# Performance work log

Measured on AMD Instinct MI355X. Metric: run time of the kernel, lower is better.

The kernel has to match this reference:

```python
import jax, jax.numpy as jnp
import numpy as np

NEG = 1e9  # large negative bias used by the original code for masked positions


def setup_inputs() -> dict:
    key = jax.random.key(0)
    k1, k2, k3 = jax.random.split(key, 3)
    B, H, W, Ck, Cv = 8, 64, 64, 64, 128
    return {
        "query": jax.random.normal(k1, (B, H, W, Ck), dtype=jnp.float32),
        "key": jax.random.normal(k2, (B, H, W, Ck), dtype=jnp.float32),
        "value": jax.random.normal(k3, (B, H, W, Cv), dtype=jnp.float32),
    }


def reference(query, key, value):
    B, Hq, Wq, Ck = query.shape
    Cv = value.shape[-1]
    Nq = Hq * Wq                      # query canvas size
    Nk = key.shape[1] * key.shape[2]  # key/value canvas size

    q = query.reshape(B, Nq, Ck)
    k = key.reshape(B, Nk, Ck)
    v = value.reshape(B, Nk, Cv)

    # strictly-causal pixelSNAIL mask: pixel i may attend only to pixels j < i
    allowed = jnp.tril(jnp.ones((Nq, Nk), dtype=query.dtype), k=-1)

    # [B, Nq, Nk] scaled dot-product scores
    scores = jnp.einsum("bqc,bkc->bqk", q, k) / jnp.sqrt(jnp.asarray(Ck, query.dtype))
    scores = scores - NEG * (1.0 - allowed)

    # softmax then redundant re-mask (as in the original module)
    probs = jax.nn.softmax(scores, axis=-1) * allowed

    out = jnp.einsum("bqk,bkv->bqv", probs, v)
    return out.reshape(B, Hq, Wq, Cv)
```

## Files before the change

kernel.cpp:

```cpp
#include <hip/hip_runtime.h>
#include <hip/hip_bf16.h>

typedef unsigned short u16;
typedef unsigned int u32;
typedef __attribute__((ext_vector_type(2))) unsigned int u32x2;
typedef __attribute__((ext_vector_type(4))) unsigned int u32x4;
typedef __attribute__((ext_vector_type(4))) float f32x4;
typedef __attribute__((ext_vector_type(8))) short bf16x8;
typedef __attribute__((ext_vector_type(16))) float f32x16;

typedef __attribute__((address_space(1))) const void as1_cvoid;
typedef __attribute__((address_space(3))) void as3_void;

__device__ __forceinline__ u32 cvtpk(float lo, float hi) {
    __hip_bfloat162 h = __float22bfloat162_rn(make_float2(lo, hi));
    u32 r; __builtin_memcpy(&r, &h, 4);
    return r;
}
__device__ __forceinline__ int crow(int r, int hl) { return (r & 3) + 8 * (r >> 2) + 4 * hl; }

#define NROW 4096
#define CK 64
#define CV 128
#define TILE_U16 24576
#define WS_NEEDED (8u * 32u * 49152u)
#define SWK(R, o) ((((R) << 7) + (o)) ^ (((R) & 7) << 4))
#define SWVG(R) ((((R) >> 3) & 15) ^ (((R) & 7) << 1))
#define SWV(R, o) ((((R) << 8) + (o)) ^ (SWVG(R) << 4))

__global__ __launch_bounds__(512, 2) void prep_k(const float* __restrict__ Kg,
                                                 const float* __restrict__ Vg,
                                                 u16* __restrict__ ws) {
    int bid = blockIdx.x;
    int b = bid >> 5, jt = bid & 31;
    int t = threadIdx.x;
    int jK = t >> 2, kc4 = t & 3;
    int vg = t & 15, jgrp = t >> 4;
    const float* Kp = Kg + ((size_t)b * NROW + jt * 128) * CK;
    const float* Vp = Vg + ((size_t)b * NROW + jt * 128) * CV;
    u16* img = ws + (size_t)(b * 32 + jt) * TILE_U16;

    {
        const float* kp = Kp + (size_t)jK * CK + kc4 * 16;
        f32x4 a0 = *(const f32x4*)kp,       a1 = *(const f32x4*)(kp + 4);
        f32x4 a2 = *(const f32x4*)(kp + 8), a3 = *(const f32x4*)(kp + 12);
        u32x4 kk0, kk1;
        kk0[0] = cvtpk(a0[0], a0[1]); kk0[1] = cvtpk(a0[2], a0[3]);
        kk0[2] = cvtpk(a1[0], a1[1]); kk0[3] = cvtpk(a1[2], a1[3]);
        kk1[0] = cvtpk(a2[0], a2[1]); kk1[1] = cvtpk(a2[2], a2[3]);
        kk1[2] = cvtpk(a3[0], a3[1]); kk1[3] = cvtpk(a3[2], a3[3]);
        *(u32x4*)&img[SWK(jK, kc4 * 32) >> 1]      = kk0;
        *(u32x4*)&img[SWK(jK, kc4 * 32 + 16) >> 1] = kk1;
    }
    {
        const float* vp = Vp + (size_t)(jgrp * 4) * CV + vg * 8;
        f32x4 va0 = *(const f32x4*)vp,            vb0 = *(const f32x4*)(vp + 4);
        f32x4 va1 = *(const f32x4*)(vp + CV),     vb1 = *(const f32x4*)(vp + CV + 4);
        f32x4 va2 = *(const f32x4*)(vp + 2 * CV), vb2 = *(const f32x4*)(vp + 2 * CV + 4);
        f32x4 va3 = *(const f32x4*)(vp + 3 * CV), vb3 = *(const f32x4*)(vp + 3 * CV + 4);
#pragma unroll
        for (int x = 0; x < 4; x++) {
            u32x2 vv;
            vv[0] = cvtpk(va0[x], va1[x]); vv[1] = cvtpk(va2[x], va3[x]);
            *(u32x2*)&img[8192 + (SWV(vg * 8 + x, jgrp * 8) >> 1)] = vv;
            vv[0] = cvtpk(vb0[x], vb1[x]); vv[1] = cvtpk(vb2[x], vb3[x]);
            *(u32x2*)&img[8192 + (SWV(vg * 8 + 4 + x, jgrp * 8) >> 1)] = vv;
        }
    }
}

__global__ __launch_bounds__(512, 2) void attn_m(const float* __restrict__ Qg,
                                                 const u16* __restrict__ ws,
                                                 float* __restrict__ O) {
    __shared__ __align__(16) u16 smem[2 * TILE_U16 + 16512];

    int bid = blockIdx.x;
    int bb = bid & 7;
    int u  = bid >> 3;
    int t  = threadIdx.x;
    int w  = t >> 6;
    int lane = t & 63;
    int ql = lane & 31, hl = lane >> 5;
    int qsub = w >> 2;
    int jq   = w & 3;
    int uL = u, uH = 63 - u;
    int NR1 = ((2 * uL + 1) >> 2) + 1;
    int NR2 = 33 - NR1;

    const float* Qp = Qg + (size_t)bb * NROW * CK;
    const u16* imgB = ws + (size_t)bb * 32 * TILE_U16;
    const float qscale = 0.125f * 1.44269504088896f;

    bf16x8 qf[4];
    auto loadQ = [&](int T) {
        const float* qb = Qp + (size_t)((T << 5) + ql) * CK;
#pragma unroll
        for (int kc = 0; kc < 4; kc++) {
            const float* qp = qb + kc * 16 + hl * 8;
            f32x4 a = *(const f32x4*)qp;
            f32x4 b2 = *(const f32x4*)(qp + 4);
            u32x4 qq;
            qq[0] = cvtpk(a[0] * qscale, a[1] * qscale);
            qq[1] = cvtpk(a[2] * qscale, a[3] * qscale);
            qq[2] = cvtpk(b2[0] * qscale, b2[1] * qscale);
            qq[3] = cvtpk(b2[2] * qscale, b2[3] * qscale);
            qf[kc] = __builtin_bit_cast(bf16x8, qq);
        }
    };
    int T_cur = 2 * uL + qsub;
    loadQ(T_cur);

    f32x16 acc[4];
#pragma unroll
    for (int vs = 0; vs < 4; vs++)
#pragma unroll
        for (int r = 0; r < 16; r++) acc[vs][r] = 0.f;
    float l = 0.f;

    auto issueTile = [&](int img_tile, int buf_u16) {
        const char* src = (const char*)(imgB + (size_t)img_tile * TILE_U16)
                          + w * 6144 + lane * 16;
        char* dst = (char*)smem + (size_t)buf_u16 * 2 + w * 6144;
#pragma unroll
        for (int i = 0; i < 6; i++)
            __builtin_amdgcn_global_load_lds((as1_cvoid*)(src + i * 1024),
                                             (as3_void*)(dst + i * 1024), 16, 0, 0);
    };

    auto combine = [&](int Tq) {
        float* cm = (float*)&smem[2 * TILE_U16];
        float* lA = cm + 8192;
        float lw = l + __shfl_xor(l, 32);
        if (jq == 0) {
#pragma unroll
            for (int vs = 0; vs < 4; vs++)
#pragma unroll
                for (int r = 0; r < 16; r++)
                    cm[qsub * 4096 + crow(r, hl) * 128 + vs * 32 + ql] = acc[vs][r];
            if (lane < 32) lA[qsub * 32 + lane] = lw;
        }
        __syncthreads();
        if (jq == 1) {
#pragma unroll
            for (int vs = 0; vs < 4; vs++)
#pragma unroll
                for (int r = 0; r < 16; r++)
                    cm[qsub * 4096 + crow(r, hl) * 128 + vs * 32 + ql] += acc[vs][r];
            if (lane < 32) lA[qsub * 32 + lane] += lw;
        }
        __syncthreads();
        if (jq == 2) {
#pragma unroll
            for (int vs = 0; vs < 4; vs++)
#pragma unroll
                for (int r = 0; r < 16; r++)
                    cm[qsub * 4096 + crow(r, hl) * 128 + vs * 32 + ql] += acc[vs][r];
            if (lane < 32) lA[qsub * 32 + lane] += lw;
        }
        __syncthreads();
        if (jq == 3) {
            float ltot = lA[qsub * 32 + ql] + lw;
            float inv = ((Tq << 5) + ql == 0) ? 0.f : 1.f / ltot;
            float inv_r[16];
#pragma unroll
            for (int r = 0; r < 16; r++) inv_r[r] = __shfl(inv, crow(r, hl));
            float* Og = O + ((size_t)bb * NROW + ((size_t)Tq << 5)) * CV;
#pragma unroll
            for (int vs = 0; vs < 4; vs++)
#pragma unroll
                for (int r = 0; r < 16; r++)
                    Og[(size_t)crow(r, hl) * CV + vs * 32 + ql] =
                        (cm[qsub * 4096 + crow(r, hl) * 128 + vs * 32 + ql] + acc[vs][r]) * inv_r[r];
        }
        __syncthreads();
    };

    issueTile(0, 0);

    for (int rr = 0; rr < 33; ++rr) {
        int cur = (rr & 1) * TILE_U16;
        int nxt = ((rr + 1) & 1) * TILE_U16;

        {
            int nr = rr + 1;
            int jb = (nr < NR1) ? nr : (nr - NR1 < NR2 ? nr - NR1 : NR2 - 1);
            issueTile(jb, nxt);
        }
        asm volatile("s_waitcnt vmcnt(6)" ::: "memory");
        __builtin_amdgcn_sched_barrier(0);
        __builtin_amdgcn_s_barrier();

        if (rr == NR1) {
            combine(T_cur);
#pragma unroll
            for (int vs = 0; vs < 4; vs++)
#pragma unroll
                for (int r = 0; r < 16; r++) acc[vs][r] = 0.f;
            l = 0.f;
            T_cur = 2 * uH + qsub;
            loadQ(T_cur);
        }

        int tt = (rr < NR1) ? rr : rr - NR1;
        int jS = 4 * tt + jq;
        if (jS <= T_cur) {
            bf16x8 kf0 = *(const bf16x8*)&smem[cur + (SWK(jq * 32 + ql, 0 * 32 + hl * 16) >> 1)];
            bf16x8 kf1 = *(const bf16x8*)&smem[cur + (SWK(jq * 32 + ql, 1 * 32 + hl * 16) >> 1)];
            bf16x8 kf2 = *(const bf16x8*)&smem[cur + (SWK(jq * 32 + ql, 2 * 32 + hl * 16) >> 1)];
            bf16x8 kf3 = *(const bf16x8*)&smem[cur + (SWK(jq * 32 + ql, 3 * 32 + hl * 16) >> 1)];

            f32x16 Sa, Sb;
#pragma unroll
            for (int r = 0; r < 16; r++) { Sa[r] = 0.f; Sb[r] = 0.f; }
            __builtin_amdgcn_s_setprio(1);
            Sa = __builtin_amdgcn_mfma_f32_32x32x16_bf16(kf0, qf[0], Sa, 0, 0, 0);
            Sb = __builtin_amdgcn_mfma_f32_32x32x16_bf16(kf2, qf[2], Sb, 0, 0, 0);
            Sa = __builtin_amdgcn_mfma_f32_32x32x16_bf16(kf1, qf[1], Sa, 0, 0, 0);
            Sb = __builtin_amdgcn_mfma_f32_32x32x16_bf16(kf3, qf[3], Sb, 0, 0, 0);
            __builtin_amdgcn_s_setprio(0);

            float P[16];
            bool diag = (jS == T_cur);
#pragma unroll
            for (int r = 0; r < 16; r++) {
                float pr2 = __builtin_exp2f(Sa[r] + Sb[r]);
                if (diag) pr2 = (crow(r, hl) >= ql) ? 0.f : pr2;
                P[r] = pr2;
            }
            {
                float s0 = (P[0] + P[1]) + (P[2] + P[3]);
                float s1 = (P[4] + P[5]) + (P[6] + P[7]);
                float s2 = (P[8] + P[9]) + (P[10] + P[11]);
                float s3 = (P[12] + P[13]) + (P[14] + P[15]);
                l += (s0 + s1) + (s2 + s3);
            }

            u32 A0 = cvtpk(P[0], P[1]),   B0 = cvtpk(P[2], P[3]);
            u32 A1 = cvtpk(P[4], P[5]),   B1 = cvtpk(P[6], P[7]);
            u32 A2 = cvtpk(P[8], P[9]),   B2 = cvtpk(P[10], P[11]);
            u32 A3 = cvtpk(P[12], P[13]), B3 = cvtpk(P[14], P[15]);
            u32 s1 = hl ? A0 : A1, s2 = hl ? B0 : B1;
            u32 s3 = hl ? A2 : A3, s4 = hl ? B2 : B3;
            u32 r1 = (u32)__shfl_xor((int)s1, 32);
            u32 r2 = (u32)__shfl_xor((int)s2, 32);
            u32 r3 = (u32)__shfl_xor((int)s3, 32);
            u32 r4 = (u32)__shfl_xor((int)s4, 32);

            bf16x8 vf0[4], vf1[4];
#pragma unroll
            for (int vs = 0; vs < 4; vs++) {
                vf0[vs] = *(const bf16x8*)&smem[cur + 8192 + (SWV(vs * 32 + ql, jq * 64 + hl * 16) >> 1)];
                vf1[vs] = *(const bf16x8*)&smem[cur + 8192 + (SWV(vs * 32 + ql, jq * 64 + 32 + hl * 16) >> 1)];
            }
            u32x4 w0, w1;
            w0[0] = hl ? r1 : A0; w0[1] = hl ? r2 : B0;
            w0[2] = hl ? A1 : r1; w0[3] = hl ? B1 : r2;
            w1[0] = hl ? r3 : A2; w1[1] = hl ? r4 : B2;
            w1[2] = hl ? A3 : r3; w1[3] = hl ? B3 : r4;
            bf16x8 pa0 = __builtin_bit_cast(bf16x8, w0);
            bf16x8 pa1 = __builtin_bit_cast(bf16x8, w1);

            __builtin_amdgcn_s_setprio(1);
#pragma unroll
            for (int vs = 0; vs < 4; vs++)
                acc[vs] = __builtin_amdgcn_mfma_f32_32x32x16_bf16(pa0, vf0[vs], acc[vs], 0, 0, 0);
#pragma unroll
            for (int vs = 0; vs < 4; vs++)
                acc[vs] = __builtin_amdgcn_mfma_f32_32x32x16_bf16(pa1, vf1[vs], acc[vs], 0, 0, 0);
            __builtin_amdgcn_s_setprio(0);
        }
        __builtin_amdgcn_s_barrier();
    }

    combine(T_cur);
}

#define FBUF 24576
#define FVT 8192
__global__ __launch_bounds__(512, 2) void attn_fb(const float* __restrict__ Qg,
                                                  const float* __restrict__ Kg,
                                                  const float* __restrict__ Vg,
                                                  float* __restrict__ O) {
    __shared__ __align__(16) u16 smem[2 * FBUF];
    int bid = blockIdx.x;
    int bb = bid & 7;
    int u  = bid >> 3;
    int t  = threadIdx.x;
    int w  = t >> 6;
    int lane = t & 63;
    int ql = lane & 31, hl = lane >> 5;
    int qsub = w >> 2, jq = w & 3;
    int uL = u, uH = 63 - u;
    int rA = ((2 * uL + 1) >> 2) + 1;
    const float* Qp = Qg + (size_t)bb * NROW * CK;
    const float* Kp = Kg + (size_t)bb * NROW * CK;
    const float* Vp = Vg + (size_t)bb * NROW * CV;
    const float qscale = 0.125f * 1.44269504088896f;
    bf16x8 qf[4];
    auto loadQ = [&](int T) {
        const float* qb = Qp + (size_t)((T << 5) + ql) * CK;
#pragma unroll
        for (int kc = 0; kc < 4; kc++) {
            const float* qp = qb + kc * 16 + hl * 8;
            f32x4 a = *(const f32x4*)qp;
            f32x4 b2 = *(const f32x4*)(qp + 4);
            u32x4 qq;
            qq[0] = cvtpk(a[0] * qscale, a[1] * qscale);
            qq[1] = cvtpk(a[2] * qscale, a[3] * qscale);
            qq[2] = cvtpk(b2[0] * qscale, b2[1] * qscale);
            qq[3] = cvtpk(b2[2] * qscale, b2[3] * qscale);
            qf[kc] = __builtin_bit_cast(bf16x8, qq);
        }
    };
    int T_cur = 2 * uL + qsub;
    loadQ(T_cur);
    f32x16 acc[4];
#pragma unroll
    for (int vs = 0; vs < 4; vs++)
#pragma unroll
        for (int r = 0; r < 16; r++) acc[vs][r] = 0.f;
    float l = 0.f;
    int jK = t >> 2, kc4 = t & 3;
    int vg = t & 15, jgrp = t >> 4;
    const float* kSrc = Kp + (size_t)jK * CK + kc4 * 16;
    const float* vSrc = Vp + (size_t)(jgrp * 4) * CV + vg * 8;
    f32x4 kr0, kr1, kr2, kr3, va0, va1, va2, va3, vb0, vb1, vb2, vb3;
    auto prefetch = [&](int jb) {
        const float* kp = kSrc + (size_t)jb * CK;
        kr0 = *(const f32x4*)kp;       kr1 = *(const f32x4*)(kp + 4);
        kr2 = *(const f32x4*)(kp + 8); kr3 = *(const f32x4*)(kp + 12);
        const float* vp = vSrc + (size_t)jb * CV;
        va0 = *(const f32x4*)vp;            vb0 = *(const f32x4*)(vp + 4);
        va1 = *(const f32x4*)(vp + CV);     vb1 = *(const f32x4*)(vp + CV + 4);
        va2 = *(const f32x4*)(vp + 2 * CV); vb2 = *(const f32x4*)(vp + 2 * CV + 4);
        va3 = *(const f32x4*)(vp + 3 * CV); vb3 = *(const f32x4*)(vp + 3 * CV + 4);
    };
    auto store_tile = [&](int bufo) {
        u32x4 kk0, kk1;
        kk0[0] = cvtpk(kr0[0], kr0[1]); kk0[1] = cvtpk(kr0[2], kr0[3]);
        kk0[2] = cvtpk(kr1[0], kr1[1]); kk0[3] = cvtpk(kr1[2], kr1[3]);
        kk1[0] = cvtpk(kr2[0], kr2[1]); kk1[1] = cvtpk(kr2[2], kr2[3]);
        kk1[2] = cvtpk(kr3[0], kr3[1]); kk1[3] = cvtpk(kr3[2], kr3[3]);
        *(u32x4*)&smem[bufo + (SWK(jK, kc4 * 32) >> 1)]      = kk0;
        *(u32x4*)&smem[bufo + (SWK(jK, kc4 * 32 + 16) >> 1)] = kk1;
#pragma unroll
        for (int x = 0; x < 4; x++) {
            int v = vg * 8 + x;
            u32x2 vv; vv[0] = cvtpk(va0[x], va1[x]); vv[1] = cvtpk(va2[x], va3[x]);
            *(u32x2*)&smem[bufo + FVT + (SWV(v, jgrp * 8) >> 1)] = vv;
        }
#pragma unroll
        for (int x = 0; x < 4; x++) {
            int v = vg * 8 + 4 + x;
            u32x2 vv; vv[0] = cvtpk(vb0[x], vb1[x]); vv[1] = cvtpk(vb2[x], vb3[x]);
            *(u32x2*)&smem[bufo + FVT + (SWV(v, jgrp * 8) >> 1)] = vv;
        }
    };
    auto combine = [&](int scratch, int Tq) {
        float* cm = (float*)(smem + scratch);
        float* lA = cm + 8192;
        float lw = l + __shfl_xor(l, 32);
        if (jq == 0) {
#pragma unroll
            for (int vs = 0; vs < 4; vs++)
#pragma unroll
                for (int r = 0; r < 16; r++)
                    cm[qsub * 4096 + crow(r, hl) * 128 + vs * 32 + ql] = acc[vs][r];
            if (lane < 32) lA[qsub * 32 + lane] = lw;
        }
        __syncthreads();
        if (jq == 1) {
#pragma unroll
            for (int vs = 0; vs < 4; vs++)
#pragma unroll
                for (int r = 0; r < 16; r++)
                    cm[qsub * 4096 + crow(r, hl) * 128 + vs * 32 + ql] += acc[vs][r];
            if (lane < 32) lA[qsub * 32 + lane] += lw;
        }
        __syncthreads();
        if (jq == 2) {
#pragma unroll
            for (int vs = 0; vs < 4; vs++)
#pragma unroll
                for (int r = 0; r < 16; r++)
                    cm[qsub * 4096 + crow(r, hl) * 128 + vs * 32 + ql] += acc[vs][r];
            if (lane < 32) lA[qsub * 32 + lane] += lw;
        }
        __syncthreads();
        if (jq == 3) {
            float ltot = lA[qsub * 32 + ql] + lw;
            float inv = ((Tq << 5) + ql == 0) ? 0.f : 1.f / ltot;
            float inv_r[16];
#pragma unroll
            for (int r = 0; r < 16; r++) inv_r[r] = __shfl(inv, crow(r, hl));
            float* Og = O + ((size_t)bb * NROW + ((size_t)Tq << 5)) * CV;
#pragma unroll
            for (int vs = 0; vs < 4; vs++)
#pragma unroll
                for (int r = 0; r < 16; r++)
                    Og[(size_t)crow(r, hl) * CV + vs * 32 + ql] =
                        (cm[qsub * 4096 + crow(r, hl) * 128 + vs * 32 + ql] + acc[vs][r]) * inv_r[r];
        }
        __syncthreads();
    };
    prefetch(0);
    for (int rr = 0; rr < 33; ++rr) {
        int bufo = (rr & 1) * FBUF;
        store_tile(bufo);
        __syncthreads();
        if (rr == rA) {
            combine(((rA - 1) & 1) * FBUF, T_cur);
#pragma unroll
            for (int vs = 0; vs < 4; vs++)
#pragma unroll
                for (int r = 0; r < 16; r++) acc[vs][r] = 0.f;
            l = 0.f;
            T_cur = 2 * uH + qsub;
            loadQ(T_cur);
        }
        int tt = (rr < rA) ? rr : rr - rA;
        int jS = 4 * tt + jq;
        {
            int nr = rr + 1;
            int jb = (nr < rA) ? (nr << 7)
                               : ((nr <= 32 ? (nr - rA) : (32 - rA)) << 7);
            prefetch(jb);
        }
        if (jS > T_cur) continue;
        bf16x8 kf0 = *(const bf16x8*)&smem[bufo + (SWK(jq * 32 + ql, 0 * 32 + hl * 16) >> 1)];
        bf16x8 kf1 = *(const bf16x8*)&smem[bufo + (SWK(jq * 32 + ql, 1 * 32 + hl * 16) >> 1)];
        bf16x8 kf2 = *(const bf16x8*)&smem[bufo + (SWK(jq * 32 + ql, 2 * 32 + hl * 16) >> 1)];
        bf16x8 kf3 = *(const bf16x8*)&smem[bufo + (SWK(jq * 32 + ql, 3 * 32 + hl * 16) >> 1)];
        f32x16 S;
#pragma unroll
        for (int r = 0; r < 16; r++) S[r] = 0.f;
        __builtin_amdgcn_s_setprio(1);
        S = __builtin_amdgcn_mfma_f32_32x32x16_bf16(kf0, qf[0], S, 0, 0, 0);
        S = __builtin_amdgcn_mfma_f32_32x32x16_bf16(kf1, qf[1], S, 0, 0, 0);
        S = __builtin_amdgcn_mfma_f32_32x32x16_bf16(kf2, qf[2], S, 0, 0, 0);
        S = __builtin_amdgcn_mfma_f32_32x32x16_bf16(kf3, qf[3], S, 0, 0, 0);
        __builtin_amdgcn_s_setprio(0);
        float P[16];
        bool diag = (jS == T_cur);
#pragma unroll
        for (int r = 0; r < 16; r++) {
            float pr2 = __builtin_exp2f(S[r]);
            if (diag) pr2 = (crow(r, hl) >= ql) ? 0.f : pr2;
            P[r] = pr2;
        }
        {
            float s0 = (P[0] + P[1]) + (P[2] + P[3]);
            float s1 = (P[4] + P[5]) + (P[6] + P[7]);
            float s2 = (P[8] + P[9]) + (P[10] + P[11]);
            float s3 = (P[12] + P[13]) + (P[14] + P[15]);
            l += (s0 + s1) + (s2 + s3);
        }
        u32 A0 = cvtpk(P[0], P[1]),   B0 = cvtpk(P[2], P[3]);
        u32 A1 = cvtpk(P[4], P[5]),   B1 = cvtpk(P[6], P[7]);
        u32 A2 = cvtpk(P[8], P[9]),   B2 = cvtpk(P[10], P[11]);
        u32 A3 = cvtpk(P[12], P[13]), B3 = cvtpk(P[14], P[15]);
        u32 s1 = hl ? A0 : A1, s2 = hl ? B0 : B1;
        u32 s3 = hl ? A2 : A3, s4 = hl ? B2 : B3;
        u32 r1 = (u32)__shfl_xor((int)s1, 32);
        u32 r2 = (u32)__shfl_xor((int)s2, 32);
        u32 r3 = (u32)__shfl_xor((int)s3, 32);
        u32 r4 = (u32)__shfl_xor((int)s4, 32);
        bf16x8 vf0[4], vf1[4];
#pragma unroll
        for (int vs = 0; vs < 4; vs++) {
            vf0[vs] = *(const bf16x8*)&smem[bufo + FVT + (SWV(vs * 32 + ql, jq * 64 + hl * 16) >> 1)];
            vf1[vs] = *(const bf16x8*)&smem[bufo + FVT + (SWV(vs * 32 + ql, jq * 64 + 32 + hl * 16) >> 1)];
        }
        u32x4 w0, w1;
        w0[0] = hl ? r1 : A0; w0[1] = hl ? r2 : B0;
        w0[2] = hl ? A1 : r1; w0[3] = hl ? B1 : r2;
        w1[0] = hl ? r3 : A2; w1[1] = hl ? r4 : B2;
        w1[2] = hl ? A3 : r3; w1[3] = hl ? B3 : r4;
        bf16x8 pa0 = __builtin_bit_cast(bf16x8, w0);
        bf16x8 pa1 = __builtin_bit_cast(bf16x8, w1);
        __builtin_amdgcn_s_setprio(1);
#pragma unroll
        for (int vs = 0; vs < 4; vs++)
            acc[vs] = __builtin_amdgcn_mfma_f32_32x32x16_bf16(pa0, vf0[vs], acc[vs], 0, 0, 0);
#pragma unroll
        for (int vs = 0; vs < 4; vs++)
            acc[vs] = __builtin_amdgcn_mfma_f32_32x32x16_bf16(pa1, vf1[vs], acc[vs], 0, 0, 0);
        __builtin_amdgcn_s_setprio(0);
    }
    __syncthreads();
    combine(0, T_cur);
}

extern "C" void kernel_launch(void* const* d_in, const int* in_sizes, int n_in,
                              void* d_out, int out_size, void* d_ws, size_t ws_size,
                              hipStream_t stream) {
    const float* Q = (const float*)d_in[0];
    const float* K = (const float*)d_in[1];
    const float* V = (const float*)d_in[2];
    float* out = (float*)d_out;
    if (ws_size >= (size_t)WS_NEEDED) {
        u16* ws = (u16*)d_ws;
        hipLaunchKernelGGL(prep_k, dim3(256), dim3(512), 0, stream, K, V, ws);
        hipLaunchKernelGGL(attn_m, dim3(256), dim3(512), 0, stream, Q, ws, out);
    } else {
        hipLaunchKernelGGL(attn_fb, dim3(256), dim3(512), 0, stream, Q, K, V, out);
    }
}
```

Before: 76.72 us.

## Split work into 512 blocks with single-query-tile pairs and V-column halves

The attention kernel now launches 512 blocks instead of 256. Each block handles one 32-row query tile from the low end paired with one from the high end, so causal work stays balanced. The eight warps now split the output columns in two halves (vh) instead of splitting across two query tiles. The K/V double buffer and its async prefetch are replaced by a single LDS buffer guarded by __syncthreads, which cuts LDS use and may allow more resident blocks. In exchange, each loaded K/V tile serves only one query tile, so global and LDS traffic roughly doubles. The QK^T MFMAs and exp are also computed twice per block (once per column half), and load latency is no longer overlapped with compute.

```diff
diff --git a/kernel.cpp b/kernel.cpp
--- a/kernel.cpp
+++ b/kernel.cpp
@@ -72,20 +72,19 @@
 __global__ __launch_bounds__(512, 2) void attn_m(const float* __restrict__ Qg,
                                                  const u16* __restrict__ ws,
                                                  float* __restrict__ O) {
-    __shared__ __align__(16) u16 smem[2 * TILE_U16 + 16512];
+    __shared__ __align__(16) u16 smem[TILE_U16 + 8320];
 
     int bid = blockIdx.x;
     int bb = bid & 7;
-    int u  = bid >> 3;
+    int p  = bid >> 3;
     int t  = threadIdx.x;
     int w  = t >> 6;
     int lane = t & 63;
     int ql = lane & 31, hl = lane >> 5;
-    int qsub = w >> 2;
-    int jq   = w & 3;
-    int uL = u, uH = 63 - u;
-    int NR1 = ((2 * uL + 1) >> 2) + 1;
-    int NR2 = 33 - NR1;
+    int jq = w & 3;
+    int vh = w >> 2;
+    int T_A = p, T_B = 127 - p;
+    int NR1 = (p >> 2) + 1;
 
     const float* Qp = Qg + (size_t)bb * NROW * CK;
     const u16* imgB = ws + (size_t)bb * 32 * TILE_U16;
@@ -107,20 +106,20 @@
             qf[kc] = __builtin_bit_cast(bf16x8, qq);
         }
     };
-    int T_cur = 2 * uL + qsub;
+    int T_cur = T_A;
     loadQ(T_cur);
 
-    f32x16 acc[4];
-#pragma unroll
-    for (int vs = 0; vs < 4; vs++)
+    f32x16 acc[2];
+#pragma unroll
+    for (int vs = 0; vs < 2; vs++)
 #pragma unroll
         for (int r = 0; r < 16; r++) acc[vs][r] = 0.f;
     float l = 0.f;
 
-    auto issueTile = [&](int img_tile, int buf_u16) {
+    auto issueTile = [&](int img_tile) {
         const char* src = (const char*)(imgB + (size_t)img_tile * TILE_U16)
                           + w * 6144 + lane * 16;
-        char* dst = (char*)smem + (size_t)buf_u16 * 2 + w * 6144;
+        char* dst = (char*)smem + w * 6144;
 #pragma unroll
         for (int i = 0; i < 6; i++)
             __builtin_amdgcn_global_load_lds((as1_cvoid*)(src + i * 1024),
@@ -128,150 +127,142 @@
     };
 
     auto combine = [&](int Tq) {
-        float* cm = (float*)&smem[2 * TILE_U16];
-        float* lA = cm + 8192;
+        float* cm = (float*)&smem[TILE_U16];
+        float* lA = cm + 4096;
         float lw = l + __shfl_xor(l, 32);
+        int cb = vh * 2048;
         if (jq == 0) {
 #pragma unroll
-            for (int vs = 0; vs < 4; vs++)
-#pragma unroll
-                for (int r = 0; r < 16; r++)
-                    cm[qsub * 4096 + crow(r, hl) * 128 + vs * 32 + ql] = acc[vs][r];
-            if (lane < 32) lA[qsub * 32 + lane] = lw;
+            for (int vs = 0; vs < 2; vs++)
+#pragma unroll
+                for (int r = 0; r < 16; r++)
+                    cm[cb + crow(r, hl) * 64 + vs * 32 + ql] = acc[vs][r];
+            if (lane < 32) lA[vh * 32 + lane] = lw;
         }
         __syncthreads();
         if (jq == 1) {
 #pragma unroll
-            for (int vs = 0; vs < 4; vs++)
-#pragma unroll
-                for (int r = 0; r < 16; r++)
-                    cm[qsub * 4096 + crow(r, hl) * 128 + vs * 32 + ql] += acc[vs][r];
-            if (lane < 32) lA[qsub * 32 + lane] += lw;
+            for (int vs = 0; vs < 2; vs++)
+#pragma unroll
+                for (int r = 0; r < 16; r++)
+                    cm[cb + crow(r, hl) * 64 + vs * 32 + ql] += acc[vs][r];
+            if (lane < 32) lA[vh * 32 + lane] += lw;
         }
         __syncthreads();
         if (jq == 2) {
 #pragma unroll
-            for (int vs = 0; vs < 4; vs++)
-#pragma unroll
-                for (int r = 0; r < 16; r++)
-                    cm[qsub * 4096 + crow(r, hl) * 128 + vs * 32 + ql] += acc[vs][r];
-            if (lane < 32) lA[qsub * 32 + lane] += lw;
+            for (int vs = 0; vs < 2; vs++)
+#pragma unroll
+                for (int r = 0; r < 16; r++)
+                    cm[cb + crow(r, hl) * 64 + vs * 32 + ql] += acc[vs][r];
+            if (lane < 32) lA[vh * 32 + lane] += lw;
         }
         __syncthreads();
         if (jq == 3) {
-            float ltot = lA[qsub * 32 + ql] + lw;
+            float ltot = lA[vh * 32 + ql] + lw;
             float inv = ((Tq << 5) + ql == 0) ? 0.f : 1.f / ltot;
             float inv_r[16];
 #pragma unroll
             for (int r = 0; r < 16; r++) inv_r[r] = __shfl(inv, crow(r, hl));
-            float* Og = O + ((size_t)bb * NROW + ((size_t)Tq << 5)) * CV;
-#pragma unroll
-            for (int vs = 0; vs < 4; vs++)
+            float* Og = O + ((size_t)bb * NROW + ((size_t)Tq << 5)) * CV + vh * 64;
+#pragma unroll
+            for (int vs = 0; vs < 2; vs++)
 #pragma unroll
                 for (int r = 0; r < 16; r++)
                     Og[(size_t)crow(r, hl) * CV + vs * 32 + ql] =
-                        (cm[qsub * 4096 + crow(r, hl) * 128 + vs * 32 + ql] + acc[vs][r]) * inv_r[r];
-        }
-        __syncthreads();
-    };
-
-    issueTile(0, 0);
+                        (cm[cb + crow(r, hl) * 64 + vs * 32 + ql] + acc[vs][r]) * inv_r[r];
+        }
+        __syncthreads();
+    };
 
     for (int rr = 0; rr < 33; ++rr) {
-        int cur = (rr & 1) * TILE_U16;
-        int nxt = ((rr + 1) & 1) * TILE_U16;
-
-        {
-            int nr = rr + 1;
-            int jb = (nr < NR1) ? nr : (nr - NR1 < NR2 ? nr - NR1 : NR2 - 1);
-            issueTile(jb, nxt);
-        }
-        asm volatile("s_waitcnt vmcnt(6)" ::: "memory");
-        __builtin_amdgcn_sched_barrier(0);
-        __builtin_amdgcn_s_barrier();
+        __syncthreads();
+        int tt = (rr < NR1) ? rr : rr - NR1;
+        issueTile(tt);
 
         if (rr == NR1) {
             combine(T_cur);
 #pragma unroll
-            for (int vs = 0; vs < 4; vs++)
+            for (int vs = 0; vs < 2; vs++)
 #pragma unroll
                 for (int r = 0; r < 16; r++) acc[vs][r] = 0.f;
             l = 0.f;
-            T_cur = 2 * uH + qsub;
+            T_cur = T_B;
             loadQ(T_cur);
         }
-
-        int tt = (rr < NR1) ? rr : rr - NR1;
+        __syncthreads();
+
         int jS = 4 * tt + jq;
-        if (jS <= T_cur) {
-            bf16x8 kf0 = *(const bf16x8*)&smem[cur + (SWK(jq * 32 + ql, 0 * 32 + hl * 16) >> 1)];
-            bf16x8 kf1 = *(const bf16x8*)&smem[cur + (SWK(jq * 32 + ql, 1 * 32 + hl * 16) >> 1)];
-            bf16x8 kf2 = *(const bf16x8*)&smem[cur + (SWK(jq * 32 + ql, 2 * 32 + hl * 16) >> 1)];
-            bf16x8 kf3 = *(const bf16x8*)&smem[cur + (SWK(jq * 32 + ql, 3 * 32 + hl * 16) >> 1)];
-
-            f32x16 Sa, Sb;
-#pragma unroll
-            for (int r = 0; r < 16; r++) { Sa[r] = 0.f; Sb[r] = 0.f; }
-            __builtin_amdgcn_s_setprio(1);
-            Sa = __builtin_amdgcn_mfma_f32_32x32x16_bf16(kf0, qf[0], Sa, 0, 0, 0);
-            Sb = __builtin_amdgcn_mfma_f32_32x32x16_bf16(kf2, qf[2], Sb, 0, 0, 0);
-            Sa = __builtin_amdgcn_mfma_f32_32x32x16_bf16(kf1, qf[1], Sa, 0, 0, 0);
-            Sb = __builtin_amdgcn_mfma_f32_32x32x16_bf16(kf3, qf[3], Sb, 0, 0, 0);
-            __builtin_amdgcn_s_setprio(0);
-
-            float P[16];
-            bool diag = (jS == T_cur);
-#pragma unroll
-            for (int r = 0; r < 16; r++) {
-                float pr2 = __builtin_exp2f(Sa[r] + Sb[r]);
-                if (diag) pr2 = (crow(r, hl) >= ql) ? 0.f : pr2;
-                P[r] = pr2;
-            }
-            {
-                float s0 = (P[0] + P[1]) + (P[2] + P[3]);
-                float s1 = (P[4] + P[5]) + (P[6] + P[7]);
-                float s2 = (P[8] + P[9]) + (P[10] + P[11]);
-                float s3 = (P[12] + P[13]) + (P[14] + P[15]);
-                l += (s0 + s1) + (s2 + s3);
-            }
-
-            u32 A0 = cvtpk(P[0], P[1]),   B0 = cvtpk(P[2], P[3]);
-            u32 A1 = cvtpk(P[4], P[5]),   B1 = cvtpk(P[6], P[7]);
-            u32 A2 = cvtpk(P[8], P[9]),   B2 = cvtpk(P[10], P[11]);
-            u32 A3 = cvtpk(P[12], P[13]), B3 = cvtpk(P[14], P[15]);
-            u32 s1 = hl ? A0 : A1, s2 = hl ? B0 : B1;
-            u32 s3 = hl ? A2 : A3, s4 = hl ? B2 : B3;
-            u32 r1 = (u32)__shfl_xor((int)s1, 32);
-            u32 r2 = (u32)__shfl_xor((int)s2, 32);
-            u32 r3 = (u32)__shfl_xor((int)s3, 32);
-            u32 r4 = (u32)__shfl_xor((int)s4, 32);
-
-            bf16x8 vf0[4], vf1[4];
-#pragma unroll
-            for (int vs = 0; vs < 4; vs++) {
-                vf0[vs] = *(const bf16x8*)&smem[cur + 8192 + (SWV(vs * 32 + ql, jq * 64 + hl * 16) >> 1)];
-                vf1[vs] = *(const bf16x8*)&smem[cur + 8192 + (SWV(vs * 32 + ql, jq * 64 + 32 + hl * 16) >> 1)];
-            }
-            u32x4 w0, w1;
-            w0[0] = hl ? r1 : A0; w0[1] = hl ? r2 : B0;
-            w0[2] = hl ? A1 : r1; w0[3] = hl ? B1 : r2;
-            w1[0] = hl ? r3 : A2; w1[1] = hl ? r4 : B2;
-            w1[2] = hl ? A3 : r3; w1[3] = hl ? B3 : r4;
-            bf16x8 pa0 = __builtin_bit_cast(bf16x8, w0);
-            bf16x8 pa1 = __builtin_bit_cast(bf16x8, w1);
-
-            __builtin_amdgcn_s_setprio(1);
-#pragma unroll
-            for (int vs = 0; vs < 4; vs++)
-                acc[vs] = __builtin_amdgcn_mfma_f32_32x32x16_bf16(pa0, vf0[vs], acc[vs], 0, 0, 0);
-#pragma unroll
-            for (int vs = 0; vs < 4; vs++)
-                acc[vs] = __builtin_amdgcn_mfma_f32_32x32x16_bf16(pa1, vf1[vs], acc[vs], 0, 0, 0);
-            __builtin_amdgcn_s_setprio(0);
-        }
-        __builtin_amdgcn_s_barrier();
+        if (jS > T_cur) continue;
+
+        bf16x8 kf0 = *(const bf16x8*)&smem[SWK(jq * 32 + ql, 0 * 32 + hl * 16) >> 1];
+        bf16x8 kf1 = *(const bf16x8*)&smem[SWK(jq * 32 + ql, 1 * 32 + hl * 16) >> 1];
+        bf16x8 kf2 = *(const bf16x8*)&smem[SWK(jq * 32 + ql, 2 * 32 + hl * 16) >> 1];
+        bf16x8 kf3 = *(const bf16x8*)&smem[SWK(jq * 32 + ql, 3 * 32 + hl * 16) >> 1];
+
+        f32x16 Sa, Sb;
+#pragma unroll
+        for (int r = 0; r < 16; r++) { Sa[r] = 0.f; Sb[r] = 0.f; }
+        __builtin_amdgcn_s_setprio(1);
+        Sa = __builtin_amdgcn_mfma_f32_32x32x16_bf16(kf0, qf[0], Sa, 0, 0, 0);
+        Sb = __builtin_amdgcn_mfma_f32_32x32x16_bf16(kf2, qf[2], Sb, 0, 0, 0);
+        Sa = __builtin_amdgcn_mfma_f32_32x32x16_bf16(kf1, qf[1], Sa, 0, 0, 0);
+        Sb = __builtin_amdgcn_mfma_f32_32x32x16_bf16(kf3, qf[3], Sb, 0, 0, 0);
+        __builtin_amdgcn_s_setprio(0);
+
+        float P[16];
+        bool diag = (jS == T_cur);
+#pragma unroll
+        for (int r = 0; r < 16; r++) {
+            float pr2 = __builtin_exp2f(Sa[r] + Sb[r]);
+            if (diag) pr2 = (crow(r, hl) >= ql) ? 0.f : pr2;
+            P[r] = pr2;
+        }
+        {
+            float s0 = (P[0] + P[1]) + (P[2] + P[3]);
+            float s1 = (P[4] + P[5]) + (P[6] + P[7]);
+            float s2 = (P[8] + P[9]) + (P[10] + P[11]);
+            float s3 = (P[12] + P[13]) + (P[14] + P[15]);
+            l += (s0 + s1) + (s2 + s3);
+        }
+
+        u32 A0 = cvtpk(P[0], P[1]),   B0 = cvtpk(P[2], P[3]);
+        u32 A1 = cvtpk(P[4], P[5]),   B1 = cvtpk(P[6], P[7]);
+        u32 A2 = cvtpk(P[8], P[9]),   B2 = cvtpk(P[10], P[11]);
+        u32 A3 = cvtpk(P[12], P[13]), B3 = cvtpk(P[14], P[15]);
+        u32 s1 = hl ? A0 : A1, s2 = hl ? B0 : B1;
+        u32 s3 = hl ? A2 : A3, s4 = hl ? B2 : B3;
+        u32 r1 = (u32)__shfl_xor((int)s1, 32);
+        u32 r2 = (u32)__shfl_xor((int)s2, 32);
+        u32 r3 = (u32)__shfl_xor((int)s3, 32);
+        u32 r4 = (u32)__shfl_xor((int)s4, 32);
+
+        bf16x8 vf0[2], vf1[2];
+#pragma unroll
+        for (int vs = 0; vs < 2; vs++) {
+            int vrow = vh * 64 + vs * 32 + ql;
+            vf0[vs] = *(const bf16x8*)&smem[8192 + (SWV(vrow, jq * 64 + hl * 16) >> 1)];
+            vf1[vs] = *(const bf16x8*)&smem[8192 + (SWV(vrow, jq * 64 + 32 + hl * 16) >> 1)];
+        }
+        u32x4 w0, w1;
+        w0[0] = hl ? r1 : A0; w0[1] = hl ? r2 : B0;
+        w0[2] = hl ? A1 : r1; w0[3] = hl ? B1 : r2;
+        w1[0] = hl ? r3 : A2; w1[1] = hl ? r4 : B2;
+        w1[2] = hl ? A3 : r3; w1[3] = hl ? B3 : r4;
+        bf16x8 pa0 = __builtin_bit_cast(bf16x8, w0);
+        bf16x8 pa1 = __builtin_bit_cast(bf16x8, w1);
+
+        __builtin_amdgcn_s_setprio(1);
+#pragma unroll
+        for (int vs = 0; vs < 2; vs++)
+            acc[vs] = __builtin_amdgcn_mfma_f32_32x32x16_bf16(pa0, vf0[vs], acc[vs], 0, 0, 0);
+#pragma unroll
+        for (int vs = 0; vs < 2; vs++)
+            acc[vs] = __builtin_amdgcn_mfma_f32_32x32x16_bf16(pa1, vf1[vs], acc[vs], 0, 0, 0);
+        __builtin_amdgcn_s_setprio(0);
     }
 
+    __syncthreads();
     combine(T_cur);
 }
 
@@ -501,7 +492,7 @@
     if (ws_size >= (size_t)WS_NEEDED) {
         u16* ws = (u16*)d_ws;
         hipLaunchKernelGGL(prep_k, dim3(256), dim3(512), 0, stream, K, V, ws);
-        hipLaunchKernelGGL(attn_m, dim3(256), dim3(512), 0, stream, Q, ws, out);
+        hipLaunchKernelGGL(attn_m, dim3(512), dim3(512), 0, stream, Q, ws, out);
     } else {
         hipLaunchKernelGGL(attn_fb, dim3(256), dim3(512), 0, stream, Q, K, V, out);
     }
```

Measured after the change: 132.5 us. 1.73x slower.

## Use 256-key tiles single-buffered with full block syncs instead of double-buffered 128-key tiles

Applied to the files above, without the earlier changes.

The K/V workspace tiles grow from 128 to 256 keys, so each block runs 17 rounds instead of 33 and each wave handles two key sub-tiles per round. The double-buffered async prefetch with vmcnt waits is replaced by one LDS buffer loaded and then consumed after __syncthreads, and the kernel drops to one block per CU. The aim is fewer barrier rounds and less per-round overhead. In exchange, loads no longer overlap compute and occupancy is halved.

```diff
diff --git a/kernel.cpp b/kernel.cpp
--- a/kernel.cpp
+++ b/kernel.cpp
@@ -22,57 +22,68 @@
 #define NROW 4096
 #define CK 64
 #define CV 128
-#define TILE_U16 24576
-#define WS_NEEDED (8u * 32u * 49152u)
+#define TILE_U16 49152
+#define VOFF 16384
+#define WS_NEEDED (8u * 16u * 98304u)
 #define SWK(R, o) ((((R) << 7) + (o)) ^ (((R) & 7) << 4))
 #define SWVG(R) ((((R) >> 3) & 15) ^ (((R) & 7) << 1))
-#define SWV(R, o) ((((R) << 8) + (o)) ^ (SWVG(R) << 4))
+#define SWV(R, o) ((((R) << 9) + (o)) ^ (SWVG(R) << 4))
 
 __global__ __launch_bounds__(512, 2) void prep_k(const float* __restrict__ Kg,
                                                  const float* __restrict__ Vg,
                                                  u16* __restrict__ ws) {
     int bid = blockIdx.x;
-    int b = bid >> 5, jt = bid & 31;
+    int b = bid >> 4, jt = bid & 15;
     int t = threadIdx.x;
-    int jK = t >> 2, kc4 = t & 3;
-    int vg = t & 15, jgrp = t >> 4;
-    const float* Kp = Kg + ((size_t)b * NROW + jt * 128) * CK;
-    const float* Vp = Vg + ((size_t)b * NROW + jt * 128) * CV;
-    u16* img = ws + (size_t)(b * 32 + jt) * TILE_U16;
+    const float* Kp = Kg + ((size_t)b * NROW + jt * 256) * CK;
+    const float* Vp = Vg + ((size_t)b * NROW + jt * 256) * CV;
+    u16* img = ws + (size_t)(b * 16 + jt) * TILE_U16;
 
     {
-        const float* kp = Kp + (size_t)jK * CK + kc4 * 16;
-        f32x4 a0 = *(const f32x4*)kp,       a1 = *(const f32x4*)(kp + 4);
-        f32x4 a2 = *(const f32x4*)(kp + 8), a3 = *(const f32x4*)(kp + 12);
-        u32x4 kk0, kk1;
-        kk0[0] = cvtpk(a0[0], a0[1]); kk0[1] = cvtpk(a0[2], a0[3]);
-        kk0[2] = cvtpk(a1[0], a1[1]); kk0[3] = cvtpk(a1[2], a1[3]);
-        kk1[0] = cvtpk(a2[0], a2[1]); kk1[1] = cvtpk(a2[2], a2[3]);
-        kk1[2] = cvtpk(a3[0], a3[1]); kk1[3] = cvtpk(a3[2], a3[3]);
-        *(u32x4*)&img[SWK(jK, kc4 * 32) >> 1]      = kk0;
-        *(u32x4*)&img[SWK(jK, kc4 * 32 + 16) >> 1] = kk1;
+        int jK = t & 255, hc = t >> 8;
+        const float* kp = Kp + (size_t)jK * CK + hc * 32;
+#pragma unroll
+        for (int q = 0; q < 4; q++) {
+            f32x4 a  = *(const f32x4*)(kp + q * 8);
+            f32x4 b2 = *(const f32x4*)(kp + q * 8 + 4);
+            u32x4 kk;
+            kk[0] = cvtpk(a[0], a[1]);   kk[1] = cvtpk(a[2], a[3]);
+            kk[2] = cvtpk(b2[0], b2[1]); kk[3] = cvtpk(b2[2], b2[3]);
+            *(u32x4*)&img[SWK(jK, hc * 64 + q * 16) >> 1] = kk;
+        }
     }
     {
-        const float* vp = Vp + (size_t)(jgrp * 4) * CV + vg * 8;
-        f32x4 va0 = *(const f32x4*)vp,            vb0 = *(const f32x4*)(vp + 4);
-        f32x4 va1 = *(const f32x4*)(vp + CV),     vb1 = *(const f32x4*)(vp + CV + 4);
-        f32x4 va2 = *(const f32x4*)(vp + 2 * CV), vb2 = *(const f32x4*)(vp + 2 * CV + 4);
-        f32x4 va3 = *(const f32x4*)(vp + 3 * CV), vb3 = *(const f32x4*)(vp + 3 * CV + 4);
+        int vg = t & 15, jgrp = t >> 4;
+        const float* vp = Vp + (size_t)(jgrp * 8) * CV + vg * 8;
+        f32x4 r0[8], r1[8];
+#pragma unroll
+        for (int i = 0; i < 8; i++) {
+            r0[i] = *(const f32x4*)(vp + (size_t)i * CV);
+            r1[i] = *(const f32x4*)(vp + (size_t)i * CV + 4);
+        }
 #pragma unroll
         for (int x = 0; x < 4; x++) {
-            u32x2 vv;
-            vv[0] = cvtpk(va0[x], va1[x]); vv[1] = cvtpk(va2[x], va3[x]);
-            *(u32x2*)&img[8192 + (SWV(vg * 8 + x, jgrp * 8) >> 1)] = vv;
-            vv[0] = cvtpk(vb0[x], vb1[x]); vv[1] = cvtpk(vb2[x], vb3[x]);
-            *(u32x2*)&img[8192 + (SWV(vg * 8 + 4 + x, jgrp * 8) >> 1)] = vv;
+            int v = vg * 8 + x;
+            u32x4 vv;
+            vv[0] = cvtpk(r0[0][x], r0[1][x]); vv[1] = cvtpk(r0[2][x], r0[3][x]);
+            vv[2] = cvtpk(r0[4][x], r0[5][x]); vv[3] = cvtpk(r0[6][x], r0[7][x]);
+            *(u32x4*)&img[VOFF + (SWV(v, jgrp * 16) >> 1)] = vv;
+        }
+#pragma unroll
+        for (int x = 0; x < 4; x++) {
+            int v = vg * 8 + 4 + x;
+            u32x4 vv;
+            vv[0] = cvtpk(r1[0][x], r1[1][x]); vv[1] = cvtpk(r1[2][x], r1[3][x]);
+            vv[2] = cvtpk(r1[4][x], r1[5][x]); vv[3] = cvtpk(r1[6][x], r1[7][x]);
+            *(u32x4*)&img[VOFF + (SWV(v, jgrp * 16) >> 1)] = vv;
         }
     }
 }
 
-__global__ __launch_bounds__(512, 2) void attn_m(const float* __restrict__ Qg,
+__global__ __launch_bounds__(512, 1) void attn_m(const float* __restrict__ Qg,
                                                  const u16* __restrict__ ws,
                                                  float* __restrict__ O) {
-    __shared__ __align__(16) u16 smem[2 * TILE_U16 + 16512];
+    __shared__ __align__(16) u16 smem[TILE_U16 + 16512];
 
     int bid = blockIdx.x;
     int bb = bid & 7;
@@ -83,12 +94,10 @@
     int ql = lane & 31, hl = lane >> 5;
     int qsub = w >> 2;
     int jq   = w & 3;
-    int uL = u, uH = 63 - u;
-    int NR1 = ((2 * uL + 1) >> 2) + 1;
-    int NR2 = 33 - NR1;
+    int NR1 = ((2 * u + 1) >> 3) + 1;
 
     const float* Qp = Qg + (size_t)bb * NROW * CK;
-    const u16* imgB = ws + (size_t)bb * 32 * TILE_U16;
+    const u16* imgB = ws + (size_t)bb * 16 * TILE_U16;
     const float qscale = 0.125f * 1.44269504088896f;
 
     bf16x8 qf[4];
@@ -107,7 +116,7 @@
             qf[kc] = __builtin_bit_cast(bf16x8, qq);
         }
     };
-    int T_cur = 2 * uL + qsub;
+    int T_cur = 2 * u + qsub;
     loadQ(T_cur);
 
     f32x16 acc[4];
@@ -117,18 +126,18 @@
         for (int r = 0; r < 16; r++) acc[vs][r] = 0.f;
     float l = 0.f;
 
-    auto issueTile = [&](int img_tile, int buf_u16) {
+    auto issueTile = [&](int img_tile) {
         const char* src = (const char*)(imgB + (size_t)img_tile * TILE_U16)
-                          + w * 6144 + lane * 16;
-        char* dst = (char*)smem + (size_t)buf_u16 * 2 + w * 6144;
-#pragma unroll
-        for (int i = 0; i < 6; i++)
+                          + w * 12288 + lane * 16;
+        char* dst = (char*)smem + w * 12288;
+#pragma unroll
+        for (int i = 0; i < 12; i++)
             __builtin_amdgcn_global_load_lds((as1_cvoid*)(src + i * 1024),
                                              (as3_void*)(dst + i * 1024), 16, 0, 0);
     };
 
     auto combine = [&](int Tq) {
-        float* cm = (float*)&smem[2 * TILE_U16];
+        float* cm = (float*)&smem[TILE_U16];
         float* lA = cm + 8192;
         float lw = l + __shfl_xor(l, 32);
         if (jq == 0) {
@@ -175,20 +184,9 @@
         __syncthreads();
     };
 
-    issueTile(0, 0);
-
-    for (int rr = 0; rr < 33; ++rr) {
-        int cur = (rr & 1) * TILE_U16;
-        int nxt = ((rr + 1) & 1) * TILE_U16;
-
-        {
-            int nr = rr + 1;
-            int jb = (nr < NR1) ? nr : (nr - NR1 < NR2 ? nr - NR1 : NR2 - 1);
-            issueTile(jb, nxt);
-        }
-        asm volatile("s_waitcnt vmcnt(6)" ::: "memory");
-        __builtin_amdgcn_sched_barrier(0);
-        __builtin_amdgcn_s_barrier();
+    for (int rr = 0; rr < 17; ++rr) {
+        int tt = (rr < NR1) ? rr : rr - NR1;
+        issueTile(tt);
 
         if (rr == NR1) {
             combine(T_cur);
@@ -197,17 +195,21 @@
 #pragma unroll
                 for (int r = 0; r < 16; r++) acc[vs][r] = 0.f;
             l = 0.f;
-            T_cur = 2 * uH + qsub;
+            T_cur = 2 * (63 - u) + qsub;
             loadQ(T_cur);
         }
-
-        int tt = (rr < NR1) ? rr : rr - NR1;
-        int jS = 4 * tt + jq;
-        if (jS <= T_cur) {
-            bf16x8 kf0 = *(const bf16x8*)&smem[cur + (SWK(jq * 32 + ql, 0 * 32 + hl * 16) >> 1)];
-            bf16x8 kf1 = *(const bf16x8*)&smem[cur + (SWK(jq * 32 + ql, 1 * 32 + hl * 16) >> 1)];
-            bf16x8 kf2 = *(const bf16x8*)&smem[cur + (SWK(jq * 32 + ql, 2 * 32 + hl * 16) >> 1)];
-            bf16x8 kf3 = *(const bf16x8*)&smem[cur + (SWK(jq * 32 + ql, 3 * 32 + hl * 16) >> 1)];
+        __syncthreads();
+
+#pragma unroll
+        for (int c = 0; c < 2; c++) {
+            int sl = jq + 4 * c;
+            int jS = 8 * tt + sl;
+            if (jS > T_cur) continue;
+
+            bf16x8 kf0 = *(const bf16x8*)&smem[SWK(sl * 32 + ql, 0 * 32 + hl * 16) >> 1];
+            bf16x8 kf1 = *(const bf16x8*)&smem[SWK(sl * 32 + ql, 1 * 32 + hl * 16) >> 1];
+            bf16x8 kf2 = *(const bf16x8*)&smem[SWK(sl * 32 + ql, 2 * 32 + hl * 16) >> 1];
+            bf16x8 kf3 = *(const bf16x8*)&smem[SWK(sl * 32 + ql, 3 * 32 + hl * 16) >> 1];
 
             f32x16 Sa, Sb;
 #pragma unroll
@@ -249,8 +251,8 @@
             bf16x8 vf0[4], vf1[4];
 #pragma unroll
             for (int vs = 0; vs < 4; vs++) {
-                vf0[vs] = *(const bf16x8*)&smem[cur + 8192 + (SWV(vs * 32 + ql, jq * 64 + hl * 16) >> 1)];
-                vf1[vs] = *(const bf16x8*)&smem[cur + 8192 + (SWV(vs * 32 + ql, jq * 64 + 32 + hl * 16) >> 1)];
+                vf0[vs] = *(const bf16x8*)&smem[VOFF + (SWV(vs * 32 + ql, sl * 64 + hl * 16) >> 1)];
+                vf1[vs] = *(const bf16x8*)&smem[VOFF + (SWV(vs * 32 + ql, sl * 64 + 32 + hl * 16) >> 1)];
             }
             u32x4 w0, w1;
             w0[0] = hl ? r1 : A0; w0[1] = hl ? r2 : B0;
@@ -269,7 +271,7 @@
                 acc[vs] = __builtin_amdgcn_mfma_f32_32x32x16_bf16(pa1, vf1[vs], acc[vs], 0, 0, 0);
             __builtin_amdgcn_s_setprio(0);
         }
-        __builtin_amdgcn_s_barrier();
+        __syncthreads();
     }
 
     combine(T_cur);
@@ -277,6 +279,7 @@
 
 #define FBUF 24576
 #define FVT 8192
+#define FSWV(R, o) ((((R) << 8) + (o)) ^ (SWVG(R) << 4))
 __global__ __launch_bounds__(512, 2) void attn_fb(const float* __restrict__ Qg,
                                                   const float* __restrict__ Kg,
                                                   const float* __restrict__ Vg,
@@ -347,13 +350,13 @@
         for (int x = 0; x < 4; x++) {
             int v = vg * 8 + x;
             u32x2 vv; vv[0] = cvtpk(va0[x], va1[x]); vv[1] = cvtpk(va2[x], va3[x]);
-            *(u32x2*)&smem[bufo + FVT + (SWV(v, jgrp * 8) >> 1)] = vv;
+            *(u32x2*)&smem[bufo + FVT + (FSWV(v, jgrp * 8) >> 1)] = vv;
         }
 #pragma unroll
         for (int x = 0; x < 4; x++) {
             int v = vg * 8 + 4 + x;
             u32x2 vv; vv[0] = cvtpk(vb0[x], vb1[x]); vv[1] = cvtpk(vb2[x], vb3[x]);
-            *(u32x2*)&smem[bufo + FVT + (SWV(v, jgrp * 8) >> 1)] = vv;
+            *(u32x2*)&smem[bufo + FVT + (FSWV(v, jgrp * 8) >> 1)] = vv;
         }
     };
     auto combine = [&](int scratch, int Tq) {
@@ -468,8 +471,8 @@
         bf16x8 vf0[4], vf1[4];
 #pragma unroll
         for (int vs = 0; vs < 4; vs++) {
-            vf0[vs] = *(const bf16x8*)&smem[bufo + FVT + (SWV(vs * 32 + ql, jq * 64 + hl * 16) >> 1)];
-            vf1[vs] = *(const bf16x8*)&smem[bufo + FVT + (SWV(vs * 32 + ql, jq * 64 + 32 + hl * 16) >> 1)];
+            vf0[vs] = *(const bf16x8*)&smem[bufo + FVT + (FSWV(vs * 32 + ql, jq * 64 + hl * 16) >> 1)];
+            vf1[vs] = *(const bf16x8*)&smem[bufo + FVT + (FSWV(vs * 32 + ql, jq * 64 + 32 + hl * 16) >> 1)];
         }
         u32x4 w0, w1;
         w0[0] = hl ? r1 : A0; w0[1] = hl ? r2 : B0;
@@ -500,7 +503,7 @@
     float* out = (float*)d_out;
     if (ws_size >= (size_t)WS_NEEDED) {
         u16* ws = (u16*)d_ws;
-        hipLaunchKernelGGL(prep_k, dim3(256), dim3(512), 0, stream, K, V, ws);
+        hipLaunchKernelGGL(prep_k, dim3(128), dim3(512), 0, stream, K, V, ws);
         hipLaunchKernelGGL(attn_m, dim3(256), dim3(512), 0, stream, Q, ws, out);
     } else {
         hipLaunchKernelGGL(attn_fb, dim3(256), dim3(512), 0, stream, Q, K, V, out);
```

After: 81.70 us. +6.5%, slower.

## Software-pipeline PV MFMAs one tile behind QK and lower occupancy hint

Applied to the files above, without the earlier changes.

Defers each tile's P·V MFMAs into the next loop iteration, so they run after that iteration's K fragments are loaded and can overlap the next tile's QK MFMAs and softmax. P and V fragments are held in registers across the barrier, with an explicit lgkmcnt wait so the V reads finish before the buffer is reused. Launch bounds drop from 2 to 1 wave-groups per CU to give the compiler room for the extra live registers. This costs occupancy and adds register pressure, and the pending PV is flushed before each combine.

```diff
diff --git a/kernel.cpp b/kernel.cpp
--- a/kernel.cpp
+++ b/kernel.cpp
@@ -69,7 +69,7 @@
     }
 }
 
-__global__ __launch_bounds__(512, 2) void attn_m(const float* __restrict__ Qg,
+__global__ __launch_bounds__(512, 1) void attn_m(const float* __restrict__ Qg,
                                                  const u16* __restrict__ ws,
                                                  float* __restrict__ O) {
     __shared__ __align__(16) u16 smem[2 * TILE_U16 + 16512];
@@ -117,6 +117,21 @@
         for (int r = 0; r < 16; r++) acc[vs][r] = 0.f;
     float l = 0.f;
 
+    bf16x8 pa0_h, pa1_h;
+    bf16x8 vf0_h[4], vf1_h[4];
+    bool act_prev = false;
+
+    auto doPV = [&]() {
+        __builtin_amdgcn_s_setprio(1);
+#pragma unroll
+        for (int vs = 0; vs < 4; vs++)
+            acc[vs] = __builtin_amdgcn_mfma_f32_32x32x16_bf16(pa0_h, vf0_h[vs], acc[vs], 0, 0, 0);
+#pragma unroll
+        for (int vs = 0; vs < 4; vs++)
+            acc[vs] = __builtin_amdgcn_mfma_f32_32x32x16_bf16(pa1_h, vf1_h[vs], acc[vs], 0, 0, 0);
+        __builtin_amdgcn_s_setprio(0);
+    };
+
     auto issueTile = [&](int img_tile, int buf_u16) {
         const char* src = (const char*)(imgB + (size_t)img_tile * TILE_U16)
                           + w * 6144 + lane * 16;
@@ -191,6 +206,7 @@
         __builtin_amdgcn_s_barrier();
 
         if (rr == NR1) {
+            if (act_prev) { doPV(); act_prev = false; }
             combine(T_cur);
 #pragma unroll
             for (int vs = 0; vs < 4; vs++)
@@ -203,12 +219,19 @@
 
         int tt = (rr < NR1) ? rr : rr - NR1;
         int jS = 4 * tt + jq;
-        if (jS <= T_cur) {
-            bf16x8 kf0 = *(const bf16x8*)&smem[cur + (SWK(jq * 32 + ql, 0 * 32 + hl * 16) >> 1)];
-            bf16x8 kf1 = *(const bf16x8*)&smem[cur + (SWK(jq * 32 + ql, 1 * 32 + hl * 16) >> 1)];
-            bf16x8 kf2 = *(const bf16x8*)&smem[cur + (SWK(jq * 32 + ql, 2 * 32 + hl * 16) >> 1)];
-            bf16x8 kf3 = *(const bf16x8*)&smem[cur + (SWK(jq * 32 + ql, 3 * 32 + hl * 16) >> 1)];
-
+        bool act_cur = (jS <= T_cur);
+
+        bf16x8 kf0, kf1, kf2, kf3;
+        if (act_cur) {
+            kf0 = *(const bf16x8*)&smem[cur + (SWK(jq * 32 + ql, 0 * 32 + hl * 16) >> 1)];
+            kf1 = *(const bf16x8*)&smem[cur + (SWK(jq * 32 + ql, 1 * 32 + hl * 16) >> 1)];
+            kf2 = *(const bf16x8*)&smem[cur + (SWK(jq * 32 + ql, 2 * 32 + hl * 16) >> 1)];
+            kf3 = *(const bf16x8*)&smem[cur + (SWK(jq * 32 + ql, 3 * 32 + hl * 16) >> 1)];
+        }
+
+        if (act_prev) doPV();
+
+        if (act_cur) {
             f32x16 Sa, Sb;
 #pragma unroll
             for (int r = 0; r < 16; r++) { Sa[r] = 0.f; Sb[r] = 0.f; }
@@ -246,32 +269,27 @@
             u32 r3 = (u32)__shfl_xor((int)s3, 32);
             u32 r4 = (u32)__shfl_xor((int)s4, 32);
 
-            bf16x8 vf0[4], vf1[4];
 #pragma unroll
             for (int vs = 0; vs < 4; vs++) {
-                vf0[vs] = *(const bf16x8*)&smem[cur + 8192 + (SWV(vs * 32 + ql, jq * 64 + hl * 16) >> 1)];
-                vf1[vs] = *(const bf16x8*)&smem[cur + 8192 + (SWV(vs * 32 + ql, jq * 64 + 32 + hl * 16) >> 1)];
+                vf0_h[vs] = *(const bf16x8*)&smem[cur + 8192 + (SWV(vs * 32 + ql, jq * 64 + hl * 16) >> 1)];
+                vf1_h[vs] = *(const bf16x8*)&smem[cur + 8192 + (SWV(vs * 32 + ql, jq * 64 + 32 + hl * 16) >> 1)];
             }
             u32x4 w0, w1;
             w0[0] = hl ? r1 : A0; w0[1] = hl ? r2 : B0;
             w0[2] = hl ? A1 : r1; w0[3] = hl ? B1 : r2;
             w1[0] = hl ? r3 : A2; w1[1] = hl ? r4 : B2;
             w1[2] = hl ? A3 : r3; w1[3] = hl ? B3 : r4;
-            bf16x8 pa0 = __builtin_bit_cast(bf16x8, w0);
-            bf16x8 pa1 = __builtin_bit_cast(bf16x8, w1);
-
-            __builtin_amdgcn_s_setprio(1);
-#pragma unroll
-            for (int vs = 0; vs < 4; vs++)
-                acc[vs] = __builtin_amdgcn_mfma_f32_32x32x16_bf16(pa0, vf0[vs], acc[vs], 0, 0, 0);
-#pragma unroll
-            for (int vs = 0; vs < 4; vs++)
-                acc[vs] = __builtin_amdgcn_mfma_f32_32x32x16_bf16(pa1, vf1[vs], acc[vs], 0, 0, 0);
-            __builtin_amdgcn_s_setprio(0);
-        }
+            pa0_h = __builtin_bit_cast(bf16x8, w0);
+            pa1_h = __builtin_bit_cast(bf16x8, w1);
+
+            asm volatile("s_waitcnt lgkmcnt(0)" ::: "memory");
+            __builtin_amdgcn_sched_barrier(0);
+        }
+        act_prev = act_cur;
         __builtin_amdgcn_s_barrier();
     }
 
+    if (act_prev) doPV();
     combine(T_cur);
 }
 
```

Measured after the change: 80.17 us. 1.05x slower.
